# Performance work log

Hardware: AMD Instinct MI355X
Metric: run time of the kernel (lower is better)

The kernel has to match this reference:

```python
import jax, jax.numpy as jnp
import numpy as np

D_MODEL = 1024
N_HEADS = 16
D_HEAD = D_MODEL // N_HEADS
LORA_RANK = 8
LORA_ALPHA = 16
LORA_SCALING = LORA_ALPHA / LORA_RANK
NEG_INF = -1.0e9


def setup_inputs() -> dict:
    key = jax.random.key(0)
    ks = jax.random.split(key, 8)
    B, S = 2, 2048
    s_in = 1.0 / np.sqrt(D_MODEL)
    return {
        "x": jax.random.normal(ks[0], (B, S, D_MODEL), dtype=jnp.float32),
        "attention_mask": jnp.ones((B, S), dtype=jnp.int32),
        "W_qkv_kernel": jax.random.normal(ks[1], (D_MODEL, 3 * D_MODEL), jnp.float32) * s_in,
        "W_qkv_bias": jnp.zeros((3 * D_MODEL,), jnp.float32),
        "lora_A_qkv": jax.random.normal(ks[2], (D_MODEL, LORA_RANK), jnp.float32) * 0.01,
        "lora_B_qkv": jax.random.normal(ks[3], (LORA_RANK, 3 * D_MODEL), jnp.float32) * 0.01,
        "c_proj_kernel": jax.random.normal(ks[4], (D_MODEL, D_MODEL), jnp.float32) * s_in,
        "c_proj_bias": jnp.zeros((D_MODEL,), jnp.float32),
        "lora_A_proj": jax.random.normal(ks[5], (D_MODEL, LORA_RANK), jnp.float32) * 0.01,
        "lora_B_proj": jax.random.normal(ks[6], (LORA_RANK, D_MODEL), jnp.float32) * 0.01,
    }


def reference(x, attention_mask, W_qkv_kernel, W_qkv_bias, lora_A_qkv, lora_B_qkv,
              c_proj_kernel, c_proj_bias, lora_A_proj, lora_B_proj):
    B, S, _ = x.shape
    # QKV projection + LoRA adapter
    qkv = x @ W_qkv_kernel + W_qkv_bias
    qkv = qkv + ((x @ lora_A_qkv) @ lora_B_qkv) * LORA_SCALING
    q, k, v = jnp.split(qkv, 3, axis=-1)
    # [B, H, S, Dh]
    q = q.reshape(B, S, N_HEADS, D_HEAD).transpose(0, 2, 1, 3)
    k = k.reshape(B, S, N_HEADS, D_HEAD).transpose(0, 2, 1, 3)
    v = v.reshape(B, S, N_HEADS, D_HEAD).transpose(0, 2, 1, 3)
    # raw scores [B, H, S, S]
    scores = jnp.einsum("bhqd,bhkd->bhqk", q, k)
    # padding mask applied BEFORE scaling (as in the original)
    pad = (attention_mask[:, None, None, :] == 0)
    scores = jnp.where(pad, NEG_INF, scores)
    # causal mask (lower triangular kept)
    causal = jnp.tril(jnp.ones((S, S), dtype=bool))
    scores = jnp.where(causal[None, None, :, :], scores, NEG_INF)
    # scaling applied AFTER masking (faithful to source: -1e9 also divided)
    scaled = scores / jnp.sqrt(jnp.float32(D_HEAD))
    attn = jax.nn.softmax(scaled, axis=-1)
    ctx = jnp.einsum("bhqk,bhkd->bhqd", attn, v)
    ctx = ctx.transpose(0, 2, 1, 3).reshape(B, S, D_MODEL)
    out = ctx @ c_proj_kernel + c_proj_bias
    out = out + ((ctx @ lora_A_proj) @ lora_B_proj) * LORA_SCALING
    return out
```

## Files before the change

### kernel.cpp

```cpp
#include <hip/hip_runtime.h>
#include <hip/hip_bf16.h>

#define LOG2E 1.4426950408889634f
#define MASKVAL (-1.25e8f * LOG2E)

typedef __bf16 bf16x8 __attribute__((ext_vector_type(8)));
typedef __bf16 bf16x4 __attribute__((ext_vector_type(4)));
typedef short  shortx4 __attribute__((ext_vector_type(4)));
typedef float  floatx4 __attribute__((ext_vector_type(4)));

__device__ __forceinline__ floatx4 mfma16(bf16x8 a, bf16x8 b, floatx4 c) {
  return __builtin_amdgcn_mfma_f32_16x16x32_bf16(a, b, c, 0, 0, 0);
}

__device__ __forceinline__ floatx4 mfma_pv(bf16x4 a, bf16x4 b, floatx4 c) {
#if __has_builtin(__builtin_amdgcn_mfma_f32_16x16x16_bf16)
  return __builtin_amdgcn_mfma_f32_16x16x16_bf16(a, b, c, 0, 0, 0);
#else
  shortx4 as, bs;
  __builtin_memcpy(&as, &a, 8);
  __builtin_memcpy(&bs, &b, 8);
  return __builtin_amdgcn_mfma_f32_16x16x16bf16_1k(as, bs, c, 0, 0, 0);
#endif
}

__device__ __forceinline__ void load_lds16(const __bf16* g, __bf16* l) {
  __builtin_amdgcn_global_load_lds(
      (const __attribute__((address_space(1))) void*)g,
      (__attribute__((address_space(3))) void*)l, 16, 0, 0);
}

__global__ __launch_bounds__(256)
void fold_wt2(const float* __restrict__ Wq, const float* __restrict__ Aq,
              const float* __restrict__ Bq, __bf16* __restrict__ WTq,
              const float* __restrict__ Wp, const float* __restrict__ Ap,
              const float* __restrict__ Bp, __bf16* __restrict__ WTp) {
  __shared__ float tile[64][65];
  __shared__ float sLb[8][64];
  const int bx = blockIdx.x;
  const bool isQ = bx < 48;
  const float* W  = isQ ? Wq : Wp;
  const float* La = isQ ? Aq : Ap;
  const float* Lb = isQ ? Bq : Bp;
  __bf16* WT = isQ ? WTq : WTp;
  const int ncols = isQ ? 3072 : 1024;
  const int nt = (isQ ? bx : bx - 48) * 64;
  const int kt = blockIdx.y * 64;
  const int tid = threadIdx.x;
  const int tx = tid & 63, ty = tid >> 6;

  float rLa[8];
  *(float4*)&rLa[0] = *(const float4*)(La + (size_t)(kt + tx) * 8);
  *(float4*)&rLa[4] = *(const float4*)(La + (size_t)(kt + tx) * 8 + 4);

#pragma unroll
  for (int rep = 0; rep < 2; rep++) {
    int idx = tid + rep * 256;
    sLb[idx >> 6][idx & 63] = Lb[(size_t)(idx >> 6) * ncols + nt + (idx & 63)];
  }
#pragma unroll
  for (int rep = 0; rep < 16; rep++) {
    int i = rep * 4 + ty;
    tile[i][tx] = W[(size_t)(kt + i) * ncols + nt + tx];
  }
  __syncthreads();
#pragma unroll
  for (int rep = 0; rep < 16; rep++) {
    int i = rep * 4 + ty;
    int n = nt + i, k = kt + tx;
    float acc = tile[tx][i];
#pragma unroll
    for (int r = 0; r < 8; r++)
      acc += 2.0f * rLa[r] * sLb[r][i];
    WT[(size_t)n * 1024 + k] = (__bf16)acc;
  }
}

__global__ __launch_bounds__(256)
void cast_x(const float* __restrict__ x, __bf16* __restrict__ o) {
  int i = blockIdx.x * 256 + threadIdx.x;
  float4 v = ((const float4*)x)[i];
  bf16x4 r = {(__bf16)v.x, (__bf16)v.y, (__bf16)v.z, (__bf16)v.w};
  ((bf16x4*)o)[i] = r;
}

__global__ __launch_bounds__(256)
void gemm_qkv(const __bf16* __restrict__ WT, const __bf16* __restrict__ X,
              const float* __restrict__ bias, __bf16* __restrict__ qk,
              __bf16* __restrict__ vtb) {
  const int K = 1024;
  __shared__ alignas(16) __bf16 As[128 * 64];
  __shared__ alignas(16) __bf16 Bs[128 * 64];
  const int tid = threadIdx.x;
  const int wave = tid >> 6, lane = tid & 63;
  const int wm = wave >> 1, wn = wave & 1;
  const int quad = lane >> 4, l15 = lane & 15;
  const int p0 = blockIdx.y * 128, s0 = blockIdx.x * 128;
  const int srow8 = lane >> 3, sc8 = lane & 7;
  const int sswz = sc8 ^ srow8;

  floatx4 acc[4][4] = {};

  for (int kb = 0; kb < K; kb += 64) {
    __syncthreads();
#pragma unroll
    for (int t = 0; t < 4; t++) {
      int rbase = (wave * 4 + t) * 8;
      int row = rbase + srow8;
      load_lds16(WT + (size_t)(p0 + row) * K + kb + sswz * 8, As + rbase * 64);
      load_lds16(X + (size_t)(s0 + row) * K + kb + sswz * 8, Bs + rbase * 64);
    }
    __syncthreads();
#pragma unroll
    for (int ks = 0; ks < 2; ks++) {
      bf16x8 af[4], bfv[4];
#pragma unroll
      for (int t = 0; t < 4; t++) {
        int ra = wm * 64 + t * 16 + l15;
        int rb = wn * 64 + t * 16 + l15;
        int ch = (ks * 4 + quad) ^ (l15 & 7);
        af[t]  = *(const bf16x8*)(As + ra * 64 + ch * 8);
        bfv[t] = *(const bf16x8*)(Bs + rb * 64 + ch * 8);
      }
#pragma unroll
      for (int mi = 0; mi < 4; mi++)
#pragma unroll
        for (int ni = 0; ni < 4; ni++)
          acc[mi][ni] = mfma16(af[mi], bfv[ni], acc[mi][ni]);
    }
  }

  const float qscale = (p0 < 1024) ? 0.125f * LOG2E : 1.0f;
#pragma unroll
  for (int mi = 0; mi < 4; mi++) {
#pragma unroll
    for (int ni = 0; ni < 4; ni++) {
      int pb = p0 + wm * 64 + mi * 16 + quad * 4;
      int s  = s0 + wn * 64 + ni * 16 + l15;
      int b = s >> 11, s2 = s & 2047;
      if (p0 < 2048) {
        int part = pb >> 10, h = (pb & 1023) >> 6, dhb = pb & 63;
        bf16x4 o = {(__bf16)((acc[mi][ni][0] + bias[pb]) * qscale),
                    (__bf16)((acc[mi][ni][1] + bias[pb + 1]) * qscale),
                    (__bf16)((acc[mi][ni][2] + bias[pb + 2]) * qscale),
                    (__bf16)((acc[mi][ni][3] + bias[pb + 3]) * qscale)};
        *(bf16x4*)(qk + (size_t)part * 4194304 +
                   ((size_t)((b * 16 + h) * 2048 + s2)) * 64 + dhb) = o;
      } else {
        int h = (pb & 1023) >> 6, dhb = pb & 63;
        int off = s2 & 63, t = off >> 4, qd = (off >> 2) & 3, rr = off & 3;
        int ps2 = (s2 & ~63) | ((t >> 1) * 32 + qd * 8 + (t & 1) * 4 + rr);
#pragma unroll
        for (int r = 0; r < 4; r++)
          vtb[((size_t)((b * 16 + h) * 64 + dhb + r)) * 2048 + ps2] =
              (__bf16)(acc[mi][ni][r] + bias[pb + r]);
      }
    }
  }
}

__global__ __launch_bounds__(256)
void gemm_proj(const __bf16* __restrict__ A, const __bf16* __restrict__ BT,
               const float* __restrict__ bias, float* __restrict__ Cout, int N) {
  const int K = 1024;
  __shared__ alignas(16) __bf16 As[64 * 64];
  __shared__ alignas(16) __bf16 Bs[128 * 64];
  const int tid = threadIdx.x;
  const int wave = tid >> 6, lane = tid & 63;
  const int wm = wave >> 1, wn = wave & 1;
  const int quad = lane >> 4, l15 = lane & 15;
  const int m0 = blockIdx.y * 64, n0 = blockIdx.x * 128;
  const int srow8 = lane >> 3, sc8 = lane & 7;
  const int sswz = sc8 ^ srow8;

  floatx4 acc[2][4] = {};

  for (int kb = 0; kb < K; kb += 64) {
    __syncthreads();
#pragma unroll
    for (int t = 0; t < 2; t++) {
      int rbase = (wave * 2 + t) * 8;
      load_lds16(A + (size_t)(m0 + rbase + srow8) * K + kb + sswz * 8,
                 As + rbase * 64);
    }
#pragma unroll
    for (int t = 0; t < 4; t++) {
      int rbase = (wave * 4 + t) * 8;
      load_lds16(BT + (size_t)(n0 + rbase + srow8) * K + kb + sswz * 8,
                 Bs + rbase * 64);
    }
    __syncthreads();
#pragma unroll
    for (int ks = 0; ks < 2; ks++) {
      bf16x8 af[2], bfv[4];
      int ch = (ks * 4 + quad) ^ (l15 & 7);
#pragma unroll
      for (int t = 0; t < 2; t++)
        af[t] = *(const bf16x8*)(As + (wm * 32 + t * 16 + l15) * 64 + ch * 8);
#pragma unroll
      for (int t = 0; t < 4; t++)
        bfv[t] = *(const bf16x8*)(Bs + (wn * 64 + t * 16 + l15) * 64 + ch * 8);
#pragma unroll
      for (int mi = 0; mi < 2; mi++)
#pragma unroll
        for (int ni = 0; ni < 4; ni++)
          acc[mi][ni] = mfma16(af[mi], bfv[ni], acc[mi][ni]);
    }
  }

#pragma unroll
  for (int mi = 0; mi < 2; mi++)
#pragma unroll
    for (int ni = 0; ni < 4; ni++) {
      int n = n0 + wn * 64 + ni * 16 + l15;
#pragma unroll
      for (int r = 0; r < 4; r++) {
        int m = m0 + wm * 32 + mi * 16 + quad * 4 + r;
        Cout[(size_t)m * N + n] = acc[mi][ni][r] + bias[n];
      }
    }
}

__global__ __launch_bounds__(256)
void flash_attn(const __bf16* __restrict__ q, const __bf16* __restrict__ k,
                const __bf16* __restrict__ vt, const int* __restrict__ amask,
                __bf16* __restrict__ ctx) {
  const int S = 2048;
  __shared__ alignas(16) __bf16 Ks[2][64 * 64];
  __shared__ alignas(16) __bf16 Vs[2][64 * 64];
  const int bid = blockIdx.x;
  const int g = bid >> 5;
  const int bh = bid & 31;
  const int u = g & 7, gq = g >> 3;
  const int jb = (gq == 0) ? 31 - u : (gq == 1) ? u : (gq == 2) ? 16 + u
                                                                : 15 - u;
  const int b = bh >> 4, h = bh & 15;
  const int wave = threadIdx.x >> 6, lane = threadIdx.x & 63;
  const int quad = lane >> 4, l15 = lane & 15;
  const int Q0 = jb * 64;
  const int qrow = Q0 + wave * 16 + l15;

  const __bf16* qp  = q  + (size_t)bh * S * 64;
  const __bf16* kp0 = k  + (size_t)bh * S * 64;
  const __bf16* vp0 = vt + (size_t)bh * 64 * S;

  const int srow8 = lane >> 3, sc8 = lane & 7;
  const int sswz = sc8 ^ srow8;

  bf16x8 qf[2];
#pragma unroll
  for (int ks = 0; ks < 2; ks++)
    qf[ks] = *(const bf16x8*)(qp + (size_t)qrow * 64 + ks * 32 + quad * 8);

  int am_cur = amask[b * S + lane];
  int am_nxt = 0;

  auto STAGE = [&](int bb, int cc) {
#pragma unroll
    for (int t = 0; t < 2; t++) {
      int rbase = (wave * 2 + t) * 8;
      load_lds16(kp0 + (size_t)cc * 4096 + (size_t)(rbase + srow8) * 64 +
                     sswz * 8,
                 &Ks[bb][rbase * 64]);
    }
#pragma unroll
    for (int t = 0; t < 2; t++) {
      int rbase = (wave * 2 + t) * 8;
      load_lds16(vp0 + (size_t)(rbase + srow8) * S + cc * 64 + sswz * 8,
                 &Vs[bb][rbase * 64]);
    }
  };

  STAGE(0, 0);

  float mrun = -1.0e30f, lrun = 0.0f;
  floatx4 oacc[4] = {};

  for (int c = 0; c <= jb; c++) {
    const int cur = c & 1;
    if (c < jb) {
      am_nxt = amask[b * S + (c + 1) * 64 + lane];
      STAGE(cur ^ 1, c + 1);
      asm volatile("s_waitcnt vmcnt(4)" ::: "memory");
    } else {
      asm volatile("s_waitcnt vmcnt(0)" ::: "memory");
    }
    __builtin_amdgcn_s_barrier();
    __builtin_amdgcn_sched_barrier(0);

    floatx4 st[4] = {};
    __builtin_amdgcn_s_setprio(1);
#pragma unroll
    for (int ks = 0; ks < 2; ks++) {
      const int ch = (ks * 4 + quad) ^ (l15 & 7);
      bf16x8 kf[4];
#pragma unroll
      for (int nt = 0; nt < 4; nt++)
        kf[nt] = *(const bf16x8*)(&Ks[cur][(nt * 16 + l15) * 64 + ch * 8]);
#pragma unroll
      for (int nt = 0; nt < 4; nt++)
        st[nt] = mfma16(kf[nt], qf[ks], st[nt]);
    }
    __builtin_amdgcn_s_setprio(0);

    unsigned long long pm = __ballot(am_cur == 0);
    if (pm == 0) {
      if (c == jb) {
#pragma unroll
        for (int nt = 0; nt < 4; nt++) {
          int kl = nt * 16 + quad * 4;
#pragma unroll
          for (int r = 0; r < 4; r++) {
            bool masked = kl + r > wave * 16 + l15;
            st[nt][r] = masked ? MASKVAL : st[nt][r];
          }
        }
      }
    } else {
#pragma unroll
      for (int nt = 0; nt < 4; nt++) {
        int kl = nt * 16 + quad * 4;
#pragma unroll
        for (int r = 0; r < 4; r++) {
          bool pad = (pm >> (kl + r)) & 1ull;
          bool masked = pad || ((c == jb) && (kl + r > wave * 16 + l15));
          st[nt][r] = masked ? MASKVAL : st[nt][r];
        }
      }
    }

    {
      float m4[4];
#pragma unroll
      for (int nt = 0; nt < 4; nt++)
        m4[nt] = fmaxf(fmaxf(st[nt][0], st[nt][1]),
                       fmaxf(st[nt][2], st[nt][3]));
      float rm = fmaxf(fmaxf(m4[0], m4[1]), fmaxf(m4[2], m4[3]));
      rm = fmaxf(rm, __shfl_xor(rm, 16, 64));
      rm = fmaxf(rm, __shfl_xor(rm, 32, 64));
      if (!__all(rm - mrun <= 8.0f)) {
        float mnew = fmaxf(mrun, rm);
        float al = exp2f(mrun - mnew);
        mrun = mnew;
        lrun *= al;
#pragma unroll
        for (int nd = 0; nd < 4; nd++)
#pragma unroll
          for (int r = 0; r < 4; r++) oacc[nd][r] *= al;
      }
      float s4[4];
#pragma unroll
      for (int nt = 0; nt < 4; nt++) {
        float p0v = exp2f(st[nt][0] - mrun);
        float p1v = exp2f(st[nt][1] - mrun);
        float p2v = exp2f(st[nt][2] - mrun);
        float p3v = exp2f(st[nt][3] - mrun);
        st[nt][0] = p0v; st[nt][1] = p1v;
        st[nt][2] = p2v; st[nt][3] = p3v;
        s4[nt] = (p0v + p1v) + (p2v + p3v);
      }
      float rs = (s4[0] + s4[1]) + (s4[2] + s4[3]);
      rs += __shfl_xor(rs, 16, 64);
      rs += __shfl_xor(rs, 32, 64);
      lrun += rs;
    }

    bf16x4 pB[4];
#pragma unroll
    for (int nt = 0; nt < 4; nt++) {
      bf16x4 pk = {(__bf16)st[nt][0], (__bf16)st[nt][1],
                   (__bf16)st[nt][2], (__bf16)st[nt][3]};
      pB[nt] = pk;
    }

    __builtin_amdgcn_s_setprio(1);
#pragma unroll
    for (int tp = 0; tp < 2; tp++) {
      const int chv = (tp * 4 + quad) ^ (l15 & 7);
#pragma unroll
      for (int nd = 0; nd < 4; nd++) {
        bf16x8 v8 = *(const bf16x8*)(&Vs[cur][(nd * 16 + l15) * 64 + chv * 8]);
        bf16x4 vA0 = {v8[0], v8[1], v8[2], v8[3]};
        bf16x4 vA1 = {v8[4], v8[5], v8[6], v8[7]};
        oacc[nd] = mfma_pv(vA0, pB[2 * tp], oacc[nd]);
        oacc[nd] = mfma_pv(vA1, pB[2 * tp + 1], oacc[nd]);
      }
    }
    __builtin_amdgcn_s_setprio(0);

    am_cur = am_nxt;
    __builtin_amdgcn_s_barrier();
  }

  const float linv = 1.0f / lrun;
#pragma unroll
  for (int nd = 0; nd < 4; nd++) {
    bf16x4 o = {(__bf16)(oacc[nd][0] * linv), (__bf16)(oacc[nd][1] * linv),
                (__bf16)(oacc[nd][2] * linv), (__bf16)(oacc[nd][3] * linv)};
    *(bf16x4*)(ctx + ((size_t)(b * 2048 + qrow)) * 1024 + h * 64 + nd * 16 +
               quad * 4) = o;
  }
}

extern "C" void kernel_launch(void* const* d_in, const int* in_sizes, int n_in,
                              void* d_out, int out_size, void* d_ws, size_t ws_size,
                              hipStream_t stream) {
  const float* x  = (const float*)d_in[0];
  const int*   am = (const int*)d_in[1];
  const float* Wq = (const float*)d_in[2];
  const float* bq = (const float*)d_in[3];
  const float* Aq = (const float*)d_in[4];
  const float* Bq = (const float*)d_in[5];
  const float* Wp = (const float*)d_in[6];
  const float* bp = (const float*)d_in[7];
  const float* Ap = (const float*)d_in[8];
  const float* Bp = (const float*)d_in[9];

  __bf16* wqkvT = (__bf16*)d_ws;
  __bf16* wpT   = wqkvT + (size_t)3072 * 1024;
  __bf16* xbf   = wpT   + (size_t)1024 * 1024;
  __bf16* qbuf  = xbf   + (size_t)4096 * 1024;
  __bf16* vtbuf = qbuf  + (size_t)2 * 4194304;
  __bf16* ctxb  = vtbuf + (size_t)4194304;

  fold_wt2<<<dim3(64, 16), 256, 0, stream>>>(Wq, Aq, Bq, wqkvT,
                                             Wp, Ap, Bp, wpT);
  cast_x<<<4096, 256, 0, stream>>>(x, xbf);

  gemm_qkv<<<dim3(32, 24), 256, 0, stream>>>(wqkvT, xbf, bq, qbuf, vtbuf);
  flash_attn<<<1024, 256, 0, stream>>>(qbuf, qbuf + 4194304, vtbuf, am, ctxb);
  gemm_proj<<<dim3(8, 64), 256, 0, stream>>>(ctxb, wpT, bp, (float*)d_out, 1024);
}
```

Before: 206.3 us.

## Split each KV tile across two wave groups in flash attention, merge softmax states

The flash attention block grows to 512 threads. Two groups of four waves each process half of every 64-key tile, keeping separate running max and sum, and the two partial results are merged through LDS at the end. Each wave now does half the QK and PV MFMA work per tile, which adds parallelism at the cost of a final merge step and a larger block. The longest-first block ordering also replaces the earlier interleaved query-block schedule. The running max now starts at 0 instead of -1e30, and the per-iteration row sum is reduced across lanes only once at the end.

Measured after the change: 210.9 us. 2.2% more time.

```diff
diff --git a/kernel.cpp b/kernel.cpp
--- a/kernel.cpp
+++ b/kernel.cpp
@@ -221,32 +221,28 @@
     }
 }
 
-__global__ __launch_bounds__(256)
+__global__ __launch_bounds__(512)
 void flash_attn(const __bf16* __restrict__ q, const __bf16* __restrict__ k,
                 const __bf16* __restrict__ vt, const int* __restrict__ amask,
                 __bf16* __restrict__ ctx) {
   const int S = 2048;
-  __shared__ alignas(16) __bf16 Ks[2][64 * 64];
-  __shared__ alignas(16) __bf16 Vs[2][64 * 64];
+  __shared__ alignas(16) __bf16 smem[4][4096];
   const int bid = blockIdx.x;
-  const int g = bid >> 5;
+  const int jb = 31 - (bid >> 5);
   const int bh = bid & 31;
-  const int u = g & 7, gq = g >> 3;
-  const int jb = (gq == 0) ? 31 - u : (gq == 1) ? u : (gq == 2) ? 16 + u
-                                                                : 15 - u;
   const int b = bh >> 4, h = bh & 15;
   const int wave = threadIdx.x >> 6, lane = threadIdx.x & 63;
+  const int half = wave >> 2, qw = wave & 3;
   const int quad = lane >> 4, l15 = lane & 15;
+  const int srow8 = lane >> 3, sc8 = lane & 7;
+  const int sswz = sc8 ^ srow8;
   const int Q0 = jb * 64;
-  const int qrow = Q0 + wave * 16 + l15;
+  const int qrow = Q0 + qw * 16 + l15;
 
   const __bf16* qp  = q  + (size_t)bh * S * 64;
   const __bf16* kp0 = k  + (size_t)bh * S * 64;
   const __bf16* vp0 = vt + (size_t)bh * 64 * S;
 
-  const int srow8 = lane >> 3, sc8 = lane & 7;
-  const int sswz = sc8 ^ srow8;
-
   bf16x8 qf[2];
 #pragma unroll
   for (int ks = 0; ks < 2; ks++)
@@ -256,24 +252,17 @@
   int am_nxt = 0;
 
   auto STAGE = [&](int bb, int cc) {
-#pragma unroll
-    for (int t = 0; t < 2; t++) {
-      int rbase = (wave * 2 + t) * 8;
-      load_lds16(kp0 + (size_t)cc * 4096 + (size_t)(rbase + srow8) * 64 +
-                     sswz * 8,
-                 &Ks[bb][rbase * 64]);
-    }
-#pragma unroll
-    for (int t = 0; t < 2; t++) {
-      int rbase = (wave * 2 + t) * 8;
-      load_lds16(vp0 + (size_t)(rbase + srow8) * S + cc * 64 + sswz * 8,
-                 &Vs[bb][rbase * 64]);
-    }
+    const int rbase = wave * 8;
+    load_lds16(kp0 + (size_t)cc * 4096 + (size_t)(rbase + srow8) * 64 +
+                   sswz * 8,
+               &smem[bb][rbase * 64]);
+    load_lds16(vp0 + (size_t)(rbase + srow8) * S + cc * 64 + sswz * 8,
+               &smem[2 + bb][rbase * 64]);
   };
 
   STAGE(0, 0);
 
-  float mrun = -1.0e30f, lrun = 0.0f;
+  float mrun = 0.0f, lrun = 0.0f;
   floatx4 oacc[4] = {};
 
   for (int c = 0; c <= jb; c++) {
@@ -281,24 +270,25 @@
     if (c < jb) {
       am_nxt = amask[b * S + (c + 1) * 64 + lane];
       STAGE(cur ^ 1, c + 1);
-      asm volatile("s_waitcnt vmcnt(4)" ::: "memory");
+      asm volatile("s_waitcnt vmcnt(3)" ::: "memory");
     } else {
       asm volatile("s_waitcnt vmcnt(0)" ::: "memory");
     }
     __builtin_amdgcn_s_barrier();
     __builtin_amdgcn_sched_barrier(0);
 
-    floatx4 st[4] = {};
+    floatx4 st[2] = {};
     __builtin_amdgcn_s_setprio(1);
 #pragma unroll
     for (int ks = 0; ks < 2; ks++) {
       const int ch = (ks * 4 + quad) ^ (l15 & 7);
-      bf16x8 kf[4];
-#pragma unroll
-      for (int nt = 0; nt < 4; nt++)
-        kf[nt] = *(const bf16x8*)(&Ks[cur][(nt * 16 + l15) * 64 + ch * 8]);
-#pragma unroll
-      for (int nt = 0; nt < 4; nt++)
+      bf16x8 kf[2];
+#pragma unroll
+      for (int nt = 0; nt < 2; nt++)
+        kf[nt] = *(const bf16x8*)(&smem[cur][((half * 2 + nt) * 16 + l15) * 64 +
+                                            ch * 8]);
+#pragma unroll
+      for (int nt = 0; nt < 2; nt++)
         st[nt] = mfma16(kf[nt], qf[ks], st[nt]);
     }
     __builtin_amdgcn_s_setprio(0);
@@ -307,83 +297,75 @@
     if (pm == 0) {
       if (c == jb) {
 #pragma unroll
-        for (int nt = 0; nt < 4; nt++) {
-          int kl = nt * 16 + quad * 4;
+        for (int nt = 0; nt < 2; nt++) {
+          int kl = (half * 2 + nt) * 16 + quad * 4;
 #pragma unroll
           for (int r = 0; r < 4; r++) {
-            bool masked = kl + r > wave * 16 + l15;
+            bool masked = kl + r > qw * 16 + l15;
             st[nt][r] = masked ? MASKVAL : st[nt][r];
           }
         }
       }
     } else {
 #pragma unroll
-      for (int nt = 0; nt < 4; nt++) {
-        int kl = nt * 16 + quad * 4;
+      for (int nt = 0; nt < 2; nt++) {
+        int kl = (half * 2 + nt) * 16 + quad * 4;
 #pragma unroll
         for (int r = 0; r < 4; r++) {
           bool pad = (pm >> (kl + r)) & 1ull;
-          bool masked = pad || ((c == jb) && (kl + r > wave * 16 + l15));
+          bool masked = pad || ((c == jb) && (kl + r > qw * 16 + l15));
           st[nt][r] = masked ? MASKVAL : st[nt][r];
         }
       }
     }
 
+    floatx4 pex[2];
+#pragma unroll
+    for (int nt = 0; nt < 2; nt++)
+#pragma unroll
+      for (int r = 0; r < 4; r++)
+        pex[nt][r] = exp2f(st[nt][r] - mrun);
+    float ssum = ((pex[0][0] + pex[0][1]) + (pex[0][2] + pex[0][3])) +
+                 ((pex[1][0] + pex[1][1]) + (pex[1][2] + pex[1][3]));
+    float rm = fmaxf(fmaxf(fmaxf(st[0][0], st[0][1]),
+                           fmaxf(st[0][2], st[0][3])),
+                     fmaxf(fmaxf(st[1][0], st[1][1]),
+                           fmaxf(st[1][2], st[1][3])));
+    rm = fmaxf(rm, __shfl_xor(rm, 16, 64));
+    rm = fmaxf(rm, __shfl_xor(rm, 32, 64));
+    if (!__all(rm - mrun <= 8.0f)) {
+      float mnew = fmaxf(mrun, rm);
+      float al = exp2f(mrun - mnew);
+      mrun = mnew;
+      lrun *= al;
+      ssum *= al;
+#pragma unroll
+      for (int nt = 0; nt < 2; nt++)
+#pragma unroll
+        for (int r = 0; r < 4; r++) pex[nt][r] *= al;
+#pragma unroll
+      for (int nd = 0; nd < 4; nd++)
+#pragma unroll
+        for (int r = 0; r < 4; r++) oacc[nd][r] *= al;
+    }
+    lrun += ssum;
+
+    bf16x4 pB0 = {(__bf16)pex[0][0], (__bf16)pex[0][1],
+                  (__bf16)pex[0][2], (__bf16)pex[0][3]};
+    bf16x4 pB1 = {(__bf16)pex[1][0], (__bf16)pex[1][1],
+                  (__bf16)pex[1][2], (__bf16)pex[1][3]};
+
+    __builtin_amdgcn_s_setprio(1);
     {
-      float m4[4];
-#pragma unroll
-      for (int nt = 0; nt < 4; nt++)
-        m4[nt] = fmaxf(fmaxf(st[nt][0], st[nt][1]),
-                       fmaxf(st[nt][2], st[nt][3]));
-      float rm = fmaxf(fmaxf(m4[0], m4[1]), fmaxf(m4[2], m4[3]));
-      rm = fmaxf(rm, __shfl_xor(rm, 16, 64));
-      rm = fmaxf(rm, __shfl_xor(rm, 32, 64));
-      if (!__all(rm - mrun <= 8.0f)) {
-        float mnew = fmaxf(mrun, rm);
-        float al = exp2f(mrun - mnew);
-        mrun = mnew;
-        lrun *= al;
-#pragma unroll
-        for (int nd = 0; nd < 4; nd++)
-#pragma unroll
-          for (int r = 0; r < 4; r++) oacc[nd][r] *= al;
-      }
-      float s4[4];
-#pragma unroll
-      for (int nt = 0; nt < 4; nt++) {
-        float p0v = exp2f(st[nt][0] - mrun);
-        float p1v = exp2f(st[nt][1] - mrun);
-        float p2v = exp2f(st[nt][2] - mrun);
-        float p3v = exp2f(st[nt][3] - mrun);
-        st[nt][0] = p0v; st[nt][1] = p1v;
-        st[nt][2] = p2v; st[nt][3] = p3v;
-        s4[nt] = (p0v + p1v) + (p2v + p3v);
-      }
-      float rs = (s4[0] + s4[1]) + (s4[2] + s4[3]);
-      rs += __shfl_xor(rs, 16, 64);
-      rs += __shfl_xor(rs, 32, 64);
-      lrun += rs;
-    }
-
-    bf16x4 pB[4];
-#pragma unroll
-    for (int nt = 0; nt < 4; nt++) {
-      bf16x4 pk = {(__bf16)st[nt][0], (__bf16)st[nt][1],
-                   (__bf16)st[nt][2], (__bf16)st[nt][3]};
-      pB[nt] = pk;
-    }
-
-    __builtin_amdgcn_s_setprio(1);
-#pragma unroll
-    for (int tp = 0; tp < 2; tp++) {
-      const int chv = (tp * 4 + quad) ^ (l15 & 7);
+      const int chv = (half * 4 + quad) ^ (l15 & 7);
 #pragma unroll
       for (int nd = 0; nd < 4; nd++) {
-        bf16x8 v8 = *(const bf16x8*)(&Vs[cur][(nd * 16 + l15) * 64 + chv * 8]);
+        bf16x8 v8 =
+            *(const bf16x8*)(&smem[2 + cur][(nd * 16 + l15) * 64 + chv * 8]);
         bf16x4 vA0 = {v8[0], v8[1], v8[2], v8[3]};
         bf16x4 vA1 = {v8[4], v8[5], v8[6], v8[7]};
-        oacc[nd] = mfma_pv(vA0, pB[2 * tp], oacc[nd]);
-        oacc[nd] = mfma_pv(vA1, pB[2 * tp + 1], oacc[nd]);
+        oacc[nd] = mfma_pv(vA0, pB0, oacc[nd]);
+        oacc[nd] = mfma_pv(vA1, pB1, oacc[nd]);
       }
     }
     __builtin_amdgcn_s_setprio(0);
@@ -392,11 +374,35 @@
     __builtin_amdgcn_s_barrier();
   }
 
-  const float linv = 1.0f / lrun;
+  lrun += __shfl_xor(lrun, 16, 64);
+  lrun += __shfl_xor(lrun, 32, 64);
+
+  float* mb = (float*)smem;
+  if (half == 1) {
+#pragma unroll
+    for (int nd = 0; nd < 4; nd++)
+#pragma unroll
+      for (int r = 0; r < 4; r++)
+        mb[(qw * 18 + nd * 4 + r) * 64 + lane] = oacc[nd][r];
+    mb[(qw * 18 + 16) * 64 + lane] = mrun;
+    mb[(qw * 18 + 17) * 64 + lane] = lrun;
+  }
+  __syncthreads();
+  if (half == 1) return;
+
+  const float m1 = mb[(qw * 18 + 16) * 64 + lane];
+  const float l1 = mb[(qw * 18 + 17) * 64 + lane];
+  const float ms = fmaxf(mrun, m1);
+  const float f0 = exp2f(mrun - ms), f1 = exp2f(m1 - ms);
+  const float linv = 1.0f / (f0 * lrun + f1 * l1);
 #pragma unroll
   for (int nd = 0; nd < 4; nd++) {
-    bf16x4 o = {(__bf16)(oacc[nd][0] * linv), (__bf16)(oacc[nd][1] * linv),
-                (__bf16)(oacc[nd][2] * linv), (__bf16)(oacc[nd][3] * linv)};
+    float ov[4];
+#pragma unroll
+    for (int r = 0; r < 4; r++)
+      ov[r] = (f0 * oacc[nd][r] + f1 * mb[(qw * 18 + nd * 4 + r) * 64 + lane]) *
+              linv;
+    bf16x4 o = {(__bf16)ov[0], (__bf16)ov[1], (__bf16)ov[2], (__bf16)ov[3]};
     *(bf16x4*)(ctx + ((size_t)(b * 2048 + qrow)) * 1024 + h * 64 + nd * 16 +
                quad * 4) = o;
   }
@@ -428,6 +434,6 @@
   cast_x<<<4096, 256, 0, stream>>>(x, xbf);
 
   gemm_qkv<<<dim3(32, 24), 256, 0, stream>>>(wqkvT, xbf, bq, qbuf, vtbuf);
-  flash_attn<<<1024, 256, 0, stream>>>(qbuf, qbuf + 4194304, vtbuf, am, ctxb);
+  flash_attn<<<1024, 512, 0, stream>>>(qbuf, qbuf + 4194304, vtbuf, am, ctxb);
   gemm_proj<<<dim3(8, 64), 256, 0, stream>>>(ctxb, wpT, bp, (float*)d_out, 1024);
 }
```

## Software-pipeline QK^T of next tile with softmax/PV of current tile in flash attention

Applied to the files above, without the earlier changes.

Restructures the attention loop so the score MMA for the next key tile is issued after the PV MMA of the current tile, with K and V staged separately and prefetched further ahead. The padding check is hoisted into a single pre-pass over the mask, the row-sum reduction across lanes is deferred to the end, and the max shuffle runs only when a rescale is needed. Block scheduling is simplified to heaviest-first ordering. The intent is to overlap exp/softmax work with matrix-core work and cut per-iteration shuffles and barriers, at the cost of more registers and a pre-loop mask scan.

Result: no change. 210.3 us (+2.0%).

```diff
diff --git a/kernel.cpp b/kernel.cpp
--- a/kernel.cpp
+++ b/kernel.cpp
@@ -229,14 +229,13 @@
   __shared__ alignas(16) __bf16 Ks[2][64 * 64];
   __shared__ alignas(16) __bf16 Vs[2][64 * 64];
   const int bid = blockIdx.x;
-  const int g = bid >> 5;
+  const int jb = 31 - (bid >> 5);
   const int bh = bid & 31;
-  const int u = g & 7, gq = g >> 3;
-  const int jb = (gq == 0) ? 31 - u : (gq == 1) ? u : (gq == 2) ? 16 + u
-                                                                : 15 - u;
   const int b = bh >> 4, h = bh & 15;
   const int wave = threadIdx.x >> 6, lane = threadIdx.x & 63;
   const int quad = lane >> 4, l15 = lane & 15;
+  const int srow8 = lane >> 3, sc8 = lane & 7;
+  const int sswz = sc8 ^ srow8;
   const int Q0 = jb * 64;
   const int qrow = Q0 + wave * 16 + l15;
 
@@ -244,18 +243,7 @@
   const __bf16* kp0 = k  + (size_t)bh * S * 64;
   const __bf16* vp0 = vt + (size_t)bh * 64 * S;
 
-  const int srow8 = lane >> 3, sc8 = lane & 7;
-  const int sswz = sc8 ^ srow8;
-
-  bf16x8 qf[2];
-#pragma unroll
-  for (int ks = 0; ks < 2; ks++)
-    qf[ks] = *(const bf16x8*)(qp + (size_t)qrow * 64 + ks * 32 + quad * 8);
-
-  int am_cur = amask[b * S + lane];
-  int am_nxt = 0;
-
-  auto STAGE = [&](int bb, int cc) {
+  auto STAGE_K = [&](int bb, int cc) {
 #pragma unroll
     for (int t = 0; t < 2; t++) {
       int rbase = (wave * 2 + t) * 8;
@@ -263,6 +251,8 @@
                      sswz * 8,
                  &Ks[bb][rbase * 64]);
     }
+  };
+  auto STAGE_V = [&](int bb, int cc) {
 #pragma unroll
     for (int t = 0; t < 2; t++) {
       int rbase = (wave * 2 + t) * 8;
@@ -271,105 +261,116 @@
     }
   };
 
-  STAGE(0, 0);
-
-  float mrun = -1.0e30f, lrun = 0.0f;
+  bf16x8 qf[2];
+#pragma unroll
+  for (int ks = 0; ks < 2; ks++)
+    qf[ks] = *(const bf16x8*)(qp + (size_t)qrow * 64 + ks * 32 + quad * 8);
+
+  int anyp = 0;
+  for (int c = 0; c <= jb; c++)
+    anyp |= (amask[b * S + c * 64 + lane] == 0) ? 1 : 0;
+  const bool padded = (__ballot(anyp) != 0ull);
+
+  STAGE_K(0, 0);
+  STAGE_V(0, 0);
+  if (jb >= 1) STAGE_K(1, 1);
+  asm volatile("s_waitcnt vmcnt(0)" ::: "memory");
+  __builtin_amdgcn_s_barrier();
+  __builtin_amdgcn_sched_barrier(0);
+
+  float mrun = 0.0f, lrun = 0.0f;
   floatx4 oacc[4] = {};
-
-  for (int c = 0; c <= jb; c++) {
-    const int cur = c & 1;
-    if (c < jb) {
-      am_nxt = amask[b * S + (c + 1) * 64 + lane];
-      STAGE(cur ^ 1, c + 1);
-      asm volatile("s_waitcnt vmcnt(4)" ::: "memory");
-    } else {
-      asm volatile("s_waitcnt vmcnt(0)" ::: "memory");
-    }
-    __builtin_amdgcn_s_barrier();
-    __builtin_amdgcn_sched_barrier(0);
-
-    floatx4 st[4] = {};
-    __builtin_amdgcn_s_setprio(1);
+  floatx4 stA[4], stB[4];
+
+  {
+#pragma unroll
+    for (int nt = 0; nt < 4; nt++) stA[nt] = floatx4{0.f, 0.f, 0.f, 0.f};
 #pragma unroll
     for (int ks = 0; ks < 2; ks++) {
       const int ch = (ks * 4 + quad) ^ (l15 & 7);
       bf16x8 kf[4];
 #pragma unroll
       for (int nt = 0; nt < 4; nt++)
-        kf[nt] = *(const bf16x8*)(&Ks[cur][(nt * 16 + l15) * 64 + ch * 8]);
+        kf[nt] = *(const bf16x8*)(&Ks[0][(nt * 16 + l15) * 64 + ch * 8]);
 #pragma unroll
       for (int nt = 0; nt < 4; nt++)
-        st[nt] = mfma16(kf[nt], qf[ks], st[nt]);
-    }
-    __builtin_amdgcn_s_setprio(0);
-
-    unsigned long long pm = __ballot(am_cur == 0);
-    if (pm == 0) {
-      if (c == jb) {
-#pragma unroll
-        for (int nt = 0; nt < 4; nt++) {
-          int kl = nt * 16 + quad * 4;
-#pragma unroll
-          for (int r = 0; r < 4; r++) {
-            bool masked = kl + r > wave * 16 + l15;
-            st[nt][r] = masked ? MASKVAL : st[nt][r];
-          }
-        }
-      }
-    } else {
+        stA[nt] = mfma16(kf[nt], qf[ks], stA[nt]);
+    }
+  }
+
+  auto BODY = [&](int i, floatx4 (&CUR)[4], floatx4 (&NXT)[4]) {
+    asm volatile("s_waitcnt vmcnt(0)" ::: "memory");
+    __builtin_amdgcn_s_barrier();
+    __builtin_amdgcn_sched_barrier(0);
+    if (i < jb) {
+      STAGE_V((i + 1) & 1, i + 1);
+      if (i + 1 < jb) STAGE_K(i & 1, i + 2);
+    }
+
+    if (padded) {
+      int am_c = amask[b * S + i * 64 + lane];
+      unsigned long long pm = __ballot(am_c == 0);
 #pragma unroll
       for (int nt = 0; nt < 4; nt++) {
         int kl = nt * 16 + quad * 4;
 #pragma unroll
         for (int r = 0; r < 4; r++) {
           bool pad = (pm >> (kl + r)) & 1ull;
-          bool masked = pad || ((c == jb) && (kl + r > wave * 16 + l15));
-          st[nt][r] = masked ? MASKVAL : st[nt][r];
+          bool masked = pad || ((i == jb) && (kl + r > wave * 16 + l15));
+          CUR[nt][r] = masked ? MASKVAL : CUR[nt][r];
         }
       }
-    }
-
-    {
-      float m4[4];
+    } else if (i == jb) {
+#pragma unroll
+      for (int nt = 0; nt < 4; nt++) {
+        int kl = nt * 16 + quad * 4;
+#pragma unroll
+        for (int r = 0; r < 4; r++) {
+          bool masked = kl + r > wave * 16 + l15;
+          CUR[nt][r] = masked ? MASKVAL : CUR[nt][r];
+        }
+      }
+    }
+
+    float inm = fmaxf(
+        fmaxf(fmaxf(fmaxf(CUR[0][0], CUR[0][1]), fmaxf(CUR[0][2], CUR[0][3])),
+              fmaxf(fmaxf(CUR[1][0], CUR[1][1]), fmaxf(CUR[1][2], CUR[1][3]))),
+        fmaxf(fmaxf(fmaxf(CUR[2][0], CUR[2][1]), fmaxf(CUR[2][2], CUR[2][3])),
+              fmaxf(fmaxf(CUR[3][0], CUR[3][1]),
+                    fmaxf(CUR[3][2], CUR[3][3]))));
+#pragma unroll
+    for (int nt = 0; nt < 4; nt++)
+#pragma unroll
+      for (int r = 0; r < 4; r++)
+        CUR[nt][r] = exp2f(CUR[nt][r] - mrun);
+    float ssum = (((CUR[0][0] + CUR[0][1]) + (CUR[0][2] + CUR[0][3])) +
+                  ((CUR[1][0] + CUR[1][1]) + (CUR[1][2] + CUR[1][3]))) +
+                 (((CUR[2][0] + CUR[2][1]) + (CUR[2][2] + CUR[2][3])) +
+                  ((CUR[3][0] + CUR[3][1]) + (CUR[3][2] + CUR[3][3])));
+    if (!__all(inm - mrun <= 8.0f)) {
+      float rm = fmaxf(inm, __shfl_xor(inm, 16, 64));
+      rm = fmaxf(rm, __shfl_xor(rm, 32, 64));
+      float mnew = fmaxf(mrun, rm);
+      float al = exp2f(mrun - mnew);
+      mrun = mnew;
+      lrun *= al;
+      ssum *= al;
 #pragma unroll
       for (int nt = 0; nt < 4; nt++)
-        m4[nt] = fmaxf(fmaxf(st[nt][0], st[nt][1]),
-                       fmaxf(st[nt][2], st[nt][3]));
-      float rm = fmaxf(fmaxf(m4[0], m4[1]), fmaxf(m4[2], m4[3]));
-      rm = fmaxf(rm, __shfl_xor(rm, 16, 64));
-      rm = fmaxf(rm, __shfl_xor(rm, 32, 64));
-      if (!__all(rm - mrun <= 8.0f)) {
-        float mnew = fmaxf(mrun, rm);
-        float al = exp2f(mrun - mnew);
-        mrun = mnew;
-        lrun *= al;
-#pragma unroll
-        for (int nd = 0; nd < 4; nd++)
-#pragma unroll
-          for (int r = 0; r < 4; r++) oacc[nd][r] *= al;
-      }
-      float s4[4];
-#pragma unroll
-      for (int nt = 0; nt < 4; nt++) {
-        float p0v = exp2f(st[nt][0] - mrun);
-        float p1v = exp2f(st[nt][1] - mrun);
-        float p2v = exp2f(st[nt][2] - mrun);
-        float p3v = exp2f(st[nt][3] - mrun);
-        st[nt][0] = p0v; st[nt][1] = p1v;
-        st[nt][2] = p2v; st[nt][3] = p3v;
-        s4[nt] = (p0v + p1v) + (p2v + p3v);
-      }
-      float rs = (s4[0] + s4[1]) + (s4[2] + s4[3]);
-      rs += __shfl_xor(rs, 16, 64);
-      rs += __shfl_xor(rs, 32, 64);
-      lrun += rs;
-    }
+#pragma unroll
+        for (int r = 0; r < 4; r++) CUR[nt][r] *= al;
+#pragma unroll
+      for (int nd = 0; nd < 4; nd++)
+#pragma unroll
+        for (int r = 0; r < 4; r++) oacc[nd][r] *= al;
+    }
+    lrun += ssum;
 
     bf16x4 pB[4];
 #pragma unroll
     for (int nt = 0; nt < 4; nt++) {
-      bf16x4 pk = {(__bf16)st[nt][0], (__bf16)st[nt][1],
-                   (__bf16)st[nt][2], (__bf16)st[nt][3]};
+      bf16x4 pk = {(__bf16)CUR[nt][0], (__bf16)CUR[nt][1],
+                   (__bf16)CUR[nt][2], (__bf16)CUR[nt][3]};
       pB[nt] = pk;
     }
 
@@ -379,18 +380,43 @@
       const int chv = (tp * 4 + quad) ^ (l15 & 7);
 #pragma unroll
       for (int nd = 0; nd < 4; nd++) {
-        bf16x8 v8 = *(const bf16x8*)(&Vs[cur][(nd * 16 + l15) * 64 + chv * 8]);
+        bf16x8 v8 =
+            *(const bf16x8*)(&Vs[i & 1][(nd * 16 + l15) * 64 + chv * 8]);
         bf16x4 vA0 = {v8[0], v8[1], v8[2], v8[3]};
         bf16x4 vA1 = {v8[4], v8[5], v8[6], v8[7]};
         oacc[nd] = mfma_pv(vA0, pB[2 * tp], oacc[nd]);
         oacc[nd] = mfma_pv(vA1, pB[2 * tp + 1], oacc[nd]);
       }
     }
+    if (i < jb) {
+#pragma unroll
+      for (int nt = 0; nt < 4; nt++) NXT[nt] = floatx4{0.f, 0.f, 0.f, 0.f};
+#pragma unroll
+      for (int ks = 0; ks < 2; ks++) {
+        const int ch = (ks * 4 + quad) ^ (l15 & 7);
+        bf16x8 kf[4];
+#pragma unroll
+        for (int nt = 0; nt < 4; nt++)
+          kf[nt] = *(const bf16x8*)(&Ks[(i + 1) & 1][(nt * 16 + l15) * 64 +
+                                                     ch * 8]);
+#pragma unroll
+        for (int nt = 0; nt < 4; nt++)
+          NXT[nt] = mfma16(kf[nt], qf[ks], NXT[nt]);
+      }
+    }
     __builtin_amdgcn_s_setprio(0);
-
-    am_cur = am_nxt;
-    __builtin_amdgcn_s_barrier();
-  }
+  };
+
+  int i = 0;
+  while (true) {
+    BODY(i, stA, stB);
+    if (++i > jb) break;
+    BODY(i, stB, stA);
+    if (++i > jb) break;
+  }
+
+  lrun += __shfl_xor(lrun, 16, 64);
+  lrun += __shfl_xor(lrun, 32, 64);
 
   const float linv = 1.0f / lrun;
 #pragma unroll
```

## Precheck padding once, defer row-sum reductions, compute exp before max reduce

Applied to the files above, without the earlier changes.

The flash attention kernel now scans the attention mask once up front to decide whether any padding exists, and drops the per-chunk mask load and ballot when there is none. The softmax now computes exponentials against the running max before reducing, and only does the cross-lane max shuffle and rescale when a lane's max exceeds the threshold. Row sums are kept per lane and reduced once at the end. The block-to-query-tile order is simplified to descending by work, which drops the previous interleaved schedule. Starting mrun at 0 instead of -inf relies on the threshold check to rescale correctly, and changes the numerics of the lazy rescale.

Result: no change. 203.8 us (-1.2%).

```diff
diff --git a/kernel.cpp b/kernel.cpp
--- a/kernel.cpp
+++ b/kernel.cpp
@@ -28,6 +28,10 @@
   __builtin_amdgcn_global_load_lds(
       (const __attribute__((address_space(1))) void*)g,
       (__attribute__((address_space(3))) void*)l, 16, 0, 0);
+}
+
+__device__ __forceinline__ float max3f(float a, float b, float c) {
+  return fmaxf(a, fmaxf(b, c));
 }
 
 __global__ __launch_bounds__(256)
@@ -229,14 +233,13 @@
   __shared__ alignas(16) __bf16 Ks[2][64 * 64];
   __shared__ alignas(16) __bf16 Vs[2][64 * 64];
   const int bid = blockIdx.x;
-  const int g = bid >> 5;
+  const int jb = 31 - (bid >> 5);
   const int bh = bid & 31;
-  const int u = g & 7, gq = g >> 3;
-  const int jb = (gq == 0) ? 31 - u : (gq == 1) ? u : (gq == 2) ? 16 + u
-                                                                : 15 - u;
   const int b = bh >> 4, h = bh & 15;
   const int wave = threadIdx.x >> 6, lane = threadIdx.x & 63;
   const int quad = lane >> 4, l15 = lane & 15;
+  const int srow8 = lane >> 3, sc8 = lane & 7;
+  const int sswz = sc8 ^ srow8;
   const int Q0 = jb * 64;
   const int qrow = Q0 + wave * 16 + l15;
 
@@ -244,16 +247,18 @@
   const __bf16* kp0 = k  + (size_t)bh * S * 64;
   const __bf16* vp0 = vt + (size_t)bh * 64 * S;
 
-  const int srow8 = lane >> 3, sc8 = lane & 7;
-  const int sswz = sc8 ^ srow8;
+  int anyp = 0;
+  const int npre = (jb + 4) >> 2;
+  for (int it = 0; it < npre; it++) {
+    int4 v = *(const int4*)(amask + b * S + it * 256 + lane * 4);
+    anyp |= (v.x == 0) | (v.y == 0) | (v.z == 0) | (v.w == 0);
+  }
+  const bool padded = (__ballot(anyp) != 0ull);
 
   bf16x8 qf[2];
 #pragma unroll
   for (int ks = 0; ks < 2; ks++)
     qf[ks] = *(const bf16x8*)(qp + (size_t)qrow * 64 + ks * 32 + quad * 8);
-
-  int am_cur = amask[b * S + lane];
-  int am_nxt = 0;
 
   auto STAGE = [&](int bb, int cc) {
 #pragma unroll
@@ -273,13 +278,12 @@
 
   STAGE(0, 0);
 
-  float mrun = -1.0e30f, lrun = 0.0f;
+  float mrun = 0.0f, lrun = 0.0f;
   floatx4 oacc[4] = {};
 
   for (int c = 0; c <= jb; c++) {
     const int cur = c & 1;
     if (c < jb) {
-      am_nxt = amask[b * S + (c + 1) * 64 + lane];
       STAGE(cur ^ 1, c + 1);
       asm volatile("s_waitcnt vmcnt(4)" ::: "memory");
     } else {
@@ -303,20 +307,9 @@
     }
     __builtin_amdgcn_s_setprio(0);
 
-    unsigned long long pm = __ballot(am_cur == 0);
-    if (pm == 0) {
-      if (c == jb) {
-#pragma unroll
-        for (int nt = 0; nt < 4; nt++) {
-          int kl = nt * 16 + quad * 4;
-#pragma unroll
-          for (int r = 0; r < 4; r++) {
-            bool masked = kl + r > wave * 16 + l15;
-            st[nt][r] = masked ? MASKVAL : st[nt][r];
-          }
-        }
-      }
-    } else {
+    if (padded) {
+      int am_c = amask[b * S + c * 64 + lane];
+      unsigned long long pm = __ballot(am_c == 0);
 #pragma unroll
       for (int nt = 0; nt < 4; nt++) {
         int kl = nt * 16 + quad * 4;
@@ -327,43 +320,51 @@
           st[nt][r] = masked ? MASKVAL : st[nt][r];
         }
       }
-    }
-
-    {
-      float m4[4];
+    } else if (c == jb) {
+#pragma unroll
+      for (int nt = 0; nt < 4; nt++) {
+        int kl = nt * 16 + quad * 4;
+#pragma unroll
+        for (int r = 0; r < 4; r++) {
+          bool masked = kl + r > wave * 16 + l15;
+          st[nt][r] = masked ? MASKVAL : st[nt][r];
+        }
+      }
+    }
+
+    float t0 = max3f(st[0][0], st[0][1], st[0][2]);
+    float t1 = max3f(st[0][3], st[1][0], st[1][1]);
+    float t2 = max3f(st[1][2], st[1][3], st[2][0]);
+    float t3 = max3f(st[2][1], st[2][2], st[2][3]);
+    float t4 = max3f(st[3][0], st[3][1], st[3][2]);
+    float inm = fmaxf(max3f(t0, t1, t2), max3f(t3, t4, st[3][3]));
+#pragma unroll
+    for (int nt = 0; nt < 4; nt++)
+#pragma unroll
+      for (int r = 0; r < 4; r++)
+        st[nt][r] = exp2f(st[nt][r] - mrun);
+    float ssum = (((st[0][0] + st[0][1]) + (st[0][2] + st[0][3])) +
+                  ((st[1][0] + st[1][1]) + (st[1][2] + st[1][3]))) +
+                 (((st[2][0] + st[2][1]) + (st[2][2] + st[2][3])) +
+                  ((st[3][0] + st[3][1]) + (st[3][2] + st[3][3])));
+    if (!__all(inm - mrun <= 8.0f)) {
+      float rm = fmaxf(inm, __shfl_xor(inm, 16, 64));
+      rm = fmaxf(rm, __shfl_xor(rm, 32, 64));
+      float mnew = fmaxf(mrun, rm);
+      float al = exp2f(mrun - mnew);
+      mrun = mnew;
+      lrun *= al;
+      ssum *= al;
 #pragma unroll
       for (int nt = 0; nt < 4; nt++)
-        m4[nt] = fmaxf(fmaxf(st[nt][0], st[nt][1]),
-                       fmaxf(st[nt][2], st[nt][3]));
-      float rm = fmaxf(fmaxf(m4[0], m4[1]), fmaxf(m4[2], m4[3]));
-      rm = fmaxf(rm, __shfl_xor(rm, 16, 64));
-      rm = fmaxf(rm, __shfl_xor(rm, 32, 64));
-      if (!__all(rm - mrun <= 8.0f)) {
-        float mnew = fmaxf(mrun, rm);
-        float al = exp2f(mrun - mnew);
-        mrun = mnew;
-        lrun *= al;
-#pragma unroll
-        for (int nd = 0; nd < 4; nd++)
-#pragma unroll
-          for (int r = 0; r < 4; r++) oacc[nd][r] *= al;
-      }
-      float s4[4];
-#pragma unroll
-      for (int nt = 0; nt < 4; nt++) {
-        float p0v = exp2f(st[nt][0] - mrun);
-        float p1v = exp2f(st[nt][1] - mrun);
-        float p2v = exp2f(st[nt][2] - mrun);
-        float p3v = exp2f(st[nt][3] - mrun);
-        st[nt][0] = p0v; st[nt][1] = p1v;
-        st[nt][2] = p2v; st[nt][3] = p3v;
-        s4[nt] = (p0v + p1v) + (p2v + p3v);
-      }
-      float rs = (s4[0] + s4[1]) + (s4[2] + s4[3]);
-      rs += __shfl_xor(rs, 16, 64);
-      rs += __shfl_xor(rs, 32, 64);
-      lrun += rs;
-    }
+#pragma unroll
+        for (int r = 0; r < 4; r++) st[nt][r] *= al;
+#pragma unroll
+      for (int nd = 0; nd < 4; nd++)
+#pragma unroll
+        for (int r = 0; r < 4; r++) oacc[nd][r] *= al;
+    }
+    lrun += ssum;
 
     bf16x4 pB[4];
 #pragma unroll
@@ -379,7 +380,8 @@
       const int chv = (tp * 4 + quad) ^ (l15 & 7);
 #pragma unroll
       for (int nd = 0; nd < 4; nd++) {
-        bf16x8 v8 = *(const bf16x8*)(&Vs[cur][(nd * 16 + l15) * 64 + chv * 8]);
+        bf16x8 v8 =
+            *(const bf16x8*)(&Vs[cur][(nd * 16 + l15) * 64 + chv * 8]);
         bf16x4 vA0 = {v8[0], v8[1], v8[2], v8[3]};
         bf16x4 vA1 = {v8[4], v8[5], v8[6], v8[7]};
         oacc[nd] = mfma_pv(vA0, pB[2 * tp], oacc[nd]);
@@ -388,9 +390,11 @@
     }
     __builtin_amdgcn_s_setprio(0);
 
-    am_cur = am_nxt;
     __builtin_amdgcn_s_barrier();
   }
+
+  lrun += __shfl_xor(lrun, 16, 64);
+  lrun += __shfl_xor(lrun, 32, 64);
 
   const float linv = 1.0f / lrun;
 #pragma unroll
```
